# Performance work log

Hardware: AMD Instinct MI355X
Metric: run time of the kernel (lower is better)

Reference implementation:

```python
import jax, jax.numpy as jnp
import numpy as np

LOG_2PI = float(np.log(2.0 * np.pi))
N = 33554432  # 2**25


def setup_inputs() -> dict:
    key = jax.random.key(0)
    k1, k2, k3, k4 = jax.random.split(key, 4)
    return {
        "x": jax.random.normal(k1, (N,), dtype=jnp.float32),
        "log_sw": jax.random.normal(k2, (1,), dtype=jnp.float32),
        "log_sz": jax.random.normal(k3, (1,), dtype=jnp.float32),
        "log_sx": jax.random.normal(k4, (1,), dtype=jnp.float32),
    }


def reference(x, log_sw, log_sz, log_sx):
    # Covariance: b*J + a*I with b = sw^2, a = sz^2 + sx^2 (compound symmetric).
    # Closed-form MVN log_prob via Sherman-Morrison + matrix determinant lemma:
    #   Sigma^{-1} = I/a - (b/(a*(a+N*b))) * J
    #   logdet(Sigma) = (N-1)*log(a) + log(a + N*b)
    n = x.shape[0]
    b = jnp.exp(2.0 * log_sw[0])                      # sw^2
    a = jnp.exp(2.0 * log_sz[0]) + jnp.exp(2.0 * log_sx[0])  # sz^2 + sx^2
    s = jnp.sum(x)                                    # 1'x
    xx = jnp.dot(x, x)                                # x'x
    quad = xx / a - b * s * s / (a * (a + n * b))     # x' Sigma^{-1} x
    logdet = (n - 1) * jnp.log(a) + jnp.log(a + n * b)
    return -0.5 * (n * LOG_2PI + logdet + quad)
```

## Files before the change

### kernel.cpp

```cpp
#include <hip/hip_runtime.h>
#include <math.h>

#define NBLK 2048
#define NTHR 256

__global__ __launch_bounds__(NTHR) void grt_partial_kernel(
    const float* __restrict__ x, float2* __restrict__ part, int n4) {
    const float4* __restrict__ x4 = reinterpret_cast<const float4*>(x);
    int tid = blockIdx.x * blockDim.x + threadIdx.x;
    int stride = gridDim.x * blockDim.x;

    float s = 0.0f, q = 0.0f;
    for (int i = tid; i < n4; i += stride) {
        float4 v = x4[i];
        s += v.x + v.y + v.z + v.w;
        q = fmaf(v.x, v.x, q);
        q = fmaf(v.y, v.y, q);
        q = fmaf(v.z, v.z, q);
        q = fmaf(v.w, v.w, q);
    }

    #pragma unroll
    for (int off = 32; off > 0; off >>= 1) {
        s += __shfl_down(s, off, 64);
        q += __shfl_down(q, off, 64);
    }

    __shared__ float2 lds[NTHR / 64];
    int lane = threadIdx.x & 63;
    int wave = threadIdx.x >> 6;
    if (lane == 0) lds[wave] = make_float2(s, q);
    __syncthreads();

    if (threadIdx.x == 0) {
        float2 acc = lds[0];
        #pragma unroll
        for (int w = 1; w < NTHR / 64; ++w) {
            acc.x += lds[w].x;
            acc.y += lds[w].y;
        }
        part[blockIdx.x] = acc;
    }
}

__global__ __launch_bounds__(NTHR) void grt_final_kernel(
    const float2* __restrict__ part, int npart,
    const float* __restrict__ log_sw, const float* __restrict__ log_sz,
    const float* __restrict__ log_sx, float* __restrict__ out, float dn) {
    float s = 0.0f, q = 0.0f;
    for (int i = threadIdx.x; i < npart; i += NTHR) {
        float2 v = part[i];
        s += v.x;
        q += v.y;
    }

    #pragma unroll
    for (int off = 32; off > 0; off >>= 1) {
        s += __shfl_down(s, off, 64);
        q += __shfl_down(q, off, 64);
    }

    __shared__ float2 lds[NTHR / 64];
    int lane = threadIdx.x & 63;
    int wave = threadIdx.x >> 6;
    if (lane == 0) lds[wave] = make_float2(s, q);
    __syncthreads();

    if (threadIdx.x == 0) {
        double ss = 0.0, qq = 0.0;
        #pragma unroll
        for (int w = 0; w < NTHR / 64; ++w) {
            ss += (double)lds[w].x;
            qq += (double)lds[w].y;
        }
        double n = (double)dn;
        double b = exp(2.0 * (double)log_sw[0]);
        double a = exp(2.0 * (double)log_sz[0]) + exp(2.0 * (double)log_sx[0]);
        double quad = qq / a - b * ss * ss / (a * (a + n * b));
        double logdet = (n - 1.0) * log(a) + log(a + n * b);
        const double LOG_2PI = 1.837877066409345483560659472811;
        out[0] = (float)(-0.5 * (n * LOG_2PI + logdet + quad));
    }
}

extern "C" void kernel_launch(void* const* d_in, const int* in_sizes, int n_in,
                              void* d_out, int out_size, void* d_ws, size_t ws_size,
                              hipStream_t stream) {
    const float* x      = (const float*)d_in[0];
    const float* log_sw = (const float*)d_in[1];
    const float* log_sz = (const float*)d_in[2];
    const float* log_sx = (const float*)d_in[3];
    float* out = (float*)d_out;
    int n = in_sizes[0];
    int n4 = n >> 2;

    float2* part = (float2*)d_ws;

    grt_partial_kernel<<<NBLK, NTHR, 0, stream>>>(x, part, n4);
    grt_final_kernel<<<1, NTHR, 0, stream>>>(part, NBLK, log_sw, log_sz, log_sx,
                                             out, (float)n);
}
```

Baseline: 30.23 us.

## Fuse partial and final reduction via last-block atomic counter; unroll loads 4x

Merges the two-kernel reduction into one kernel: each block writes its partial, bumps an atomic counter, and the last block to finish does the final sum and the closed-form log-prob. The main loop also issues four independent float4 loads per iteration with separate accumulators, giving more memory-level parallelism. A hipMemsetAsync resets the counter on every call, so one kernel launch is traded for a memset, and the result now depends on threadfence/atomic ordering being correct.

```diff
diff --git a/kernel.cpp b/kernel.cpp
--- a/kernel.cpp
+++ b/kernel.cpp
@@ -3,22 +3,47 @@
 
 #define NBLK 2048
 #define NTHR 256
+#define NWAVE (NTHR / 64)
+#define COUNTER_OFF (NBLK * sizeof(float2))
 
-__global__ __launch_bounds__(NTHR) void grt_partial_kernel(
-    const float* __restrict__ x, float2* __restrict__ part, int n4) {
+__global__ __launch_bounds__(NTHR) void grt_fused_kernel(
+    const float* __restrict__ x, int n4,
+    float2* __restrict__ part, unsigned int* __restrict__ counter,
+    const float* __restrict__ log_sw, const float* __restrict__ log_sz,
+    const float* __restrict__ log_sx, float* __restrict__ out, float dn) {
     const float4* __restrict__ x4 = reinterpret_cast<const float4*>(x);
-    int tid = blockIdx.x * blockDim.x + threadIdx.x;
-    int stride = gridDim.x * blockDim.x;
+    const int tid = blockIdx.x * NTHR + threadIdx.x;
+    const int stride = gridDim.x * NTHR;
 
-    float s = 0.0f, q = 0.0f;
-    for (int i = tid; i < n4; i += stride) {
-        float4 v = x4[i];
-        s += v.x + v.y + v.z + v.w;
-        q = fmaf(v.x, v.x, q);
-        q = fmaf(v.y, v.y, q);
-        q = fmaf(v.z, v.z, q);
-        q = fmaf(v.w, v.w, q);
+    float s0 = 0.f, s1 = 0.f, s2 = 0.f, s3 = 0.f;
+    float q0 = 0.f, q1 = 0.f, q2 = 0.f, q3 = 0.f;
+    int i = tid;
+    for (; i + 3 * stride < n4; i += 4 * stride) {
+        float4 a = x4[i];
+        float4 b = x4[i + stride];
+        float4 c = x4[i + 2 * stride];
+        float4 d = x4[i + 3 * stride];
+        s0 += a.x + a.y + a.z + a.w;
+        s1 += b.x + b.y + b.z + b.w;
+        s2 += c.x + c.y + c.z + c.w;
+        s3 += d.x + d.y + d.z + d.w;
+        q0 = fmaf(a.x, a.x, q0); q0 = fmaf(a.y, a.y, q0);
+        q0 = fmaf(a.z, a.z, q0); q0 = fmaf(a.w, a.w, q0);
+        q1 = fmaf(b.x, b.x, q1); q1 = fmaf(b.y, b.y, q1);
+        q1 = fmaf(b.z, b.z, q1); q1 = fmaf(b.w, b.w, q1);
+        q2 = fmaf(c.x, c.x, q2); q2 = fmaf(c.y, c.y, q2);
+        q2 = fmaf(c.z, c.z, q2); q2 = fmaf(c.w, c.w, q2);
+        q3 = fmaf(d.x, d.x, q3); q3 = fmaf(d.y, d.y, q3);
+        q3 = fmaf(d.z, d.z, q3); q3 = fmaf(d.w, d.w, q3);
     }
+    for (; i < n4; i += stride) {
+        float4 a = x4[i];
+        s0 += a.x + a.y + a.z + a.w;
+        q0 = fmaf(a.x, a.x, q0); q0 = fmaf(a.y, a.y, q0);
+        q0 = fmaf(a.z, a.z, q0); q0 = fmaf(a.w, a.w, q0);
+    }
+    float s = (s0 + s1) + (s2 + s3);
+    float q = (q0 + q1) + (q2 + q3);
 
     #pragma unroll
     for (int off = 32; off > 0; off >>= 1) {
@@ -26,60 +51,58 @@
         q += __shfl_down(q, off, 64);
     }
 
-    __shared__ float2 lds[NTHR / 64];
-    int lane = threadIdx.x & 63;
-    int wave = threadIdx.x >> 6;
+    __shared__ float2 lds[NWAVE];
+    __shared__ int is_last;
+    const int lane = threadIdx.x & 63;
+    const int wave = threadIdx.x >> 6;
     if (lane == 0) lds[wave] = make_float2(s, q);
     __syncthreads();
 
     if (threadIdx.x == 0) {
         float2 acc = lds[0];
         #pragma unroll
-        for (int w = 1; w < NTHR / 64; ++w) {
+        for (int w = 1; w < NWAVE; ++w) {
             acc.x += lds[w].x;
             acc.y += lds[w].y;
         }
         part[blockIdx.x] = acc;
+        __threadfence();
+        unsigned int old = atomicAdd(counter, 1u);
+        is_last = (old == (unsigned int)(gridDim.x - 1));
     }
-}
-
-__global__ __launch_bounds__(NTHR) void grt_final_kernel(
-    const float2* __restrict__ part, int npart,
-    const float* __restrict__ log_sw, const float* __restrict__ log_sz,
-    const float* __restrict__ log_sx, float* __restrict__ out, float dn) {
-    float s = 0.0f, q = 0.0f;
-    for (int i = threadIdx.x; i < npart; i += NTHR) {
-        float2 v = part[i];
-        s += v.x;
-        q += v.y;
-    }
-
-    #pragma unroll
-    for (int off = 32; off > 0; off >>= 1) {
-        s += __shfl_down(s, off, 64);
-        q += __shfl_down(q, off, 64);
-    }
-
-    __shared__ float2 lds[NTHR / 64];
-    int lane = threadIdx.x & 63;
-    int wave = threadIdx.x >> 6;
-    if (lane == 0) lds[wave] = make_float2(s, q);
     __syncthreads();
 
-    if (threadIdx.x == 0) {
-        double ss = 0.0, qq = 0.0;
+    if (is_last) {
+        __threadfence();
+        float fs = 0.f, fq = 0.f;
+        for (int p = threadIdx.x; p < NBLK; p += NTHR) {
+            float2 v = part[p];
+            fs += v.x;
+            fq += v.y;
+        }
         #pragma unroll
-        for (int w = 0; w < NTHR / 64; ++w) {
-            ss += (double)lds[w].x;
-            qq += (double)lds[w].y;
+        for (int off = 32; off > 0; off >>= 1) {
+            fs += __shfl_down(fs, off, 64);
+            fq += __shfl_down(fq, off, 64);
         }
-        double n = (double)dn;
-        double b = exp(2.0 * (double)log_sw[0]);
-        double a = exp(2.0 * (double)log_sz[0]) + exp(2.0 * (double)log_sx[0]);
-        double quad = qq / a - b * ss * ss / (a * (a + n * b));
-        double logdet = (n - 1.0) * log(a) + log(a + n * b);
-        const double LOG_2PI = 1.837877066409345483560659472811;
-        out[0] = (float)(-0.5 * (n * LOG_2PI + logdet + quad));
+        __syncthreads();
+        if (lane == 0) lds[wave] = make_float2(fs, fq);
+        __syncthreads();
+        if (threadIdx.x == 0) {
+            double ss = 0.0, qq = 0.0;
+            #pragma unroll
+            for (int w = 0; w < NWAVE; ++w) {
+                ss += (double)lds[w].x;
+                qq += (double)lds[w].y;
+            }
+            double n = (double)dn;
+            double b = exp(2.0 * (double)log_sw[0]);
+            double a = exp(2.0 * (double)log_sz[0]) + exp(2.0 * (double)log_sx[0]);
+            double quad = qq / a - b * ss * ss / (a * (a + n * b));
+            double logdet = (n - 1.0) * log(a) + log(a + n * b);
+            const double LOG_2PI = 1.837877066409345483560659472811;
+            out[0] = (float)(-0.5 * (n * LOG_2PI + logdet + quad));
+        }
     }
 }
 
@@ -95,8 +118,9 @@
     int n4 = n >> 2;
 
     float2* part = (float2*)d_ws;
+    unsigned int* counter = (unsigned int*)((char*)d_ws + COUNTER_OFF);
 
-    grt_partial_kernel<<<NBLK, NTHR, 0, stream>>>(x, part, n4);
-    grt_final_kernel<<<1, NTHR, 0, stream>>>(part, NBLK, log_sw, log_sz, log_sx,
-                                             out, (float)n);
+    hipMemsetAsync(counter, 0, sizeof(unsigned int), stream);
+    grt_fused_kernel<<<NBLK, NTHR, 0, stream>>>(x, n4, part, counter, log_sw,
+                                                log_sz, log_sx, out, (float)n);
 }
```

After: 97.21 us. 222% more time.
